# Optimization experiments

Measured on AMD Instinct MI355X. Metric: run time of the kernel, lower is better.

Reference implementation:

```python
import jax, jax.numpy as jnp
import numpy as np
import math

PHI = (1 + math.sqrt(5)) / 2
ALPHA = 1 / PHI          # residual scale
BETA = 1 / PHI ** 2      # sparse-matmul scale
DIM = 1910
NZ = int(DIM * DIM / PHI)


def setup_inputs() -> dict:
    key = jax.random.key(0)
    kx, ki, kv = jax.random.split(key, 3)
    x = jax.random.normal(kx, (8, 4096, DIM), dtype=jnp.float32)
    W_indices = jax.random.randint(ki, (2, NZ), 0, DIM, dtype=jnp.int32)
    W_values = jax.random.normal(kv, (NZ,), dtype=jnp.float32) / math.sqrt(DIM)
    return {"x": x, "W_indices": W_indices, "W_values": W_values}


def reference(x, W_indices, W_values):
    dim = x.shape[-1]
    # COO -> dense: duplicate (row,col) entries sum, matching torch.sparse semantics.
    W = jnp.zeros((dim, dim), dtype=x.dtype).at[W_indices[0], W_indices[1]].add(W_values)
    orig_shape = x.shape
    xf = x.reshape(-1, dim)          # [tokens, dim]
    Wx = xf @ W.T                    # (W @ x.T).T == x @ W.T
    out = ALPHA * xf + BETA * Wx
    return out.reshape(orig_shape)
```

## Files before the change

kernel.cpp:

```cpp
#include <hip/hip_runtime.h>
#include <hip/hip_bf16.h>
#include <stdint.h>

#define DIMV 1910
#define KP   1920
#define NT   30
#define PHI_F  1.6180339887498949f
#define BETA_F 0.3819660112501051f

typedef __attribute__((ext_vector_type(4))) float f32x4;
typedef __attribute__((ext_vector_type(8))) short bf16x8;
typedef __attribute__((ext_vector_type(8))) unsigned short u16x8;

__device__ __forceinline__ void gl16(const void* g, void* l) {
    __builtin_amdgcn_global_load_lds(
        (const __attribute__((address_space(1))) void*)(uintptr_t)g,
        (__attribute__((address_space(3))) void*)(uint32_t)(uintptr_t)l,
        16, 0, 0);
}

__global__ void k_scatter(const int* __restrict__ ridx, const int* __restrict__ cidx,
                          const float* __restrict__ vals, float* __restrict__ Wd, int nz) {
    int i = blockIdx.x * 256 + threadIdx.x;
    if (i < nz) atomicAdd(Wd + (long)ridx[i] * DIMV + cidx[i], vals[i]);
}

__global__ void k_build_w(const float* __restrict__ Wd, unsigned short* __restrict__ Wb, int total8) {
    int stride = gridDim.x * blockDim.x;
    for (int i = blockIdx.x * blockDim.x + threadIdx.x; i < total8; i += stride) {
        int v = i * 8;
        int n = v / KP;
        int k = v - n * KP;
        u16x8 o;
#pragma unroll
        for (int j = 0; j < 8; ++j) {
            int kk = k + j;
            float fv = (n < DIMV && kk < DIMV) ? Wd[(size_t)n * DIMV + kk] : 0.f;
            if (kk == n && n < DIMV) fv += PHI_F;
            __hip_bfloat16 b = __float2bfloat16(fv);
            o[j] = *reinterpret_cast<unsigned short*>(&b);
        }
        *(u16x8*)(Wb + (size_t)v) = o;
    }
}

__global__ void k_conv_x(const float* __restrict__ x, unsigned short* __restrict__ xb, int total8) {
    int stride = gridDim.x * blockDim.x;
    for (int i = blockIdx.x * blockDim.x + threadIdx.x; i < total8; i += stride) {
        int v = i * 8;
        int row = v / KP;
        int col = v - row * KP;
        u16x8 o;
        if (col + 8 <= DIMV) {
            const float2* s = (const float2*)(x + (size_t)row * DIMV + col);
            float2 f0 = s[0], f1 = s[1], f2 = s[2], f3 = s[3];
            float f[8] = {f0.x, f0.y, f1.x, f1.y, f2.x, f2.y, f3.x, f3.y};
#pragma unroll
            for (int j = 0; j < 8; ++j) {
                __hip_bfloat16 b = __float2bfloat16(f[j]);
                o[j] = *reinterpret_cast<unsigned short*>(&b);
            }
        } else {
#pragma unroll
            for (int j = 0; j < 8; ++j) {
                int c = col + j;
                float fv = (c < DIMV) ? x[(size_t)row * DIMV + c] : 0.f;
                __hip_bfloat16 b = __float2bfloat16(fv);
                o[j] = *reinterpret_cast<unsigned short*>(&b);
            }
        }
        *(u16x8*)(xb + (size_t)v) = o;
    }
}

__global__ __launch_bounds__(512, 2) void k_gemm(const short* __restrict__ A,
                                                 const short* __restrict__ B,
                                                 float* __restrict__ C) {
    __shared__ short As[3 * 256 * 64];
    __shared__ short Bs[3 * 128 * 64];

    const int bid = blockIdx.x;
    const int logical = (bid & 7) * 240 + (bid >> 3);
    const int bm = logical / 15;
    const int bn = logical % 15;

    const int tid = threadIdx.x;
    const int w   = tid >> 6;
    const int l   = tid & 63;
    const int wr  = w >> 1;
    const int wc  = w & 1;
    const int fr  = l & 15;
    const int q   = l >> 4;

    const int srow  = tid >> 3;
    const int sslot = (tid & 7) ^ (srow & 7);
    const char* aG = (const char*)A + ((size_t)(bm * 256 + srow) * KP) * 2 + sslot * 16;
    const char* bG = (const char*)B + ((size_t)(bn * 128 + srow) * KP) * 2 + sslot * 16;
    const size_t gstep = (size_t)64 * KP * 2;
    char* aL = (char*)As + tid * 16;
    char* bL = (char*)Bs + tid * 16;

    const int aBase = (wr * 64 + fr) * 128;
    const int bBase = (wc * 64 + fr) * 128;
    const int co0 = ((q    ) ^ (fr & 7)) * 16;
    const int co1 = ((q + 4) ^ (fr & 7)) * 16;

    f32x4 acc[4][4] = {};

#pragma unroll
    for (int g = 0; g < 4; ++g) gl16(aG + g * gstep, aL + g * 8192);
#pragma unroll
    for (int g = 0; g < 2; ++g) gl16(bG + g * gstep, bL + g * 8192);
#pragma unroll
    for (int g = 0; g < 4; ++g) gl16(aG + 128 + g * gstep, aL + 32768 + g * 8192);
#pragma unroll
    for (int g = 0; g < 2; ++g) gl16(bG + 128 + g * gstep, bL + 16384 + g * 8192);
    asm volatile("s_waitcnt vmcnt(6)" ::: "memory");
    __builtin_amdgcn_s_barrier();
    asm volatile("" ::: "memory");

    int aRd = 0, bRd = 0;
    int aSt = 2 * 32768, bSt = 2 * 16384;

#pragma unroll 3
    for (int t = 0; t < NT; ++t) {
        const char* pa = (const char*)As + aRd + aBase;
        const char* pb = (const char*)Bs + bRd + bBase;

        bf16x8 af[4][2], b0[2][2];
#pragma unroll
        for (int mi = 0; mi < 4; ++mi) {
            af[mi][0] = *(const bf16x8*)(pa + mi * 2048 + co0);
            af[mi][1] = *(const bf16x8*)(pa + mi * 2048 + co1);
        }
#pragma unroll
        for (int ni = 0; ni < 2; ++ni) {
            b0[ni][0] = *(const bf16x8*)(pb + ni * 2048 + co0);
            b0[ni][1] = *(const bf16x8*)(pb + ni * 2048 + co1);
        }
        if (t + 2 < NT) {
            const char* g = aG + (size_t)(t + 2) * 128;
#pragma unroll
            for (int gi = 0; gi < 4; ++gi) gl16(g + gi * gstep, aL + aSt + gi * 8192);
        }
        asm volatile("" ::: "memory");
        __builtin_amdgcn_s_barrier();
        asm volatile("" ::: "memory");
        __builtin_amdgcn_s_setprio(1);
#pragma unroll
        for (int mi = 0; mi < 4; ++mi)
#pragma unroll
            for (int ni = 0; ni < 2; ++ni) {
                acc[mi][ni] = __builtin_amdgcn_mfma_f32_16x16x32_bf16(af[mi][0], b0[ni][0], acc[mi][ni], 0, 0, 0);
                acc[mi][ni] = __builtin_amdgcn_mfma_f32_16x16x32_bf16(af[mi][1], b0[ni][1], acc[mi][ni], 0, 0, 0);
            }
        __builtin_amdgcn_s_setprio(0);
        asm volatile("" ::: "memory");
        __builtin_amdgcn_s_barrier();
        asm volatile("" ::: "memory");

        bf16x8 b1[2][2];
#pragma unroll
        for (int ni = 0; ni < 2; ++ni) {
            b1[ni][0] = *(const bf16x8*)(pb + (ni + 2) * 2048 + co0);
            b1[ni][1] = *(const bf16x8*)(pb + (ni + 2) * 2048 + co1);
        }
        if (t + 2 < NT) {
            const char* g = bG + (size_t)(t + 2) * 128;
#pragma unroll
            for (int gi = 0; gi < 2; ++gi) gl16(g + gi * gstep, bL + bSt + gi * 8192);
            asm volatile("s_waitcnt vmcnt(6)" ::: "memory");
        } else {
            asm volatile("s_waitcnt vmcnt(0)" ::: "memory");
        }
        __builtin_amdgcn_s_barrier();
        asm volatile("" ::: "memory");
        __builtin_amdgcn_s_setprio(1);
#pragma unroll
        for (int mi = 0; mi < 4; ++mi)
#pragma unroll
            for (int ni = 0; ni < 2; ++ni) {
                acc[mi][ni + 2] = __builtin_amdgcn_mfma_f32_16x16x32_bf16(af[mi][0], b1[ni][0], acc[mi][ni + 2], 0, 0, 0);
                acc[mi][ni + 2] = __builtin_amdgcn_mfma_f32_16x16x32_bf16(af[mi][1], b1[ni][1], acc[mi][ni + 2], 0, 0, 0);
            }
        __builtin_amdgcn_s_setprio(0);
        asm volatile("" ::: "memory");
        __builtin_amdgcn_s_barrier();
        asm volatile("" ::: "memory");

        aRd += 32768; if (aRd == 98304) aRd = 0;
        bRd += 16384; if (bRd == 49152) bRd = 0;
        aSt += 32768; if (aSt == 98304) aSt = 0;
        bSt += 16384; if (bSt == 49152) bSt = 0;
    }

    const int grow0 = bm * 256 + wr * 64 + q * 4;
    const int gcol0 = bn * 128 + wc * 64 + fr;
#pragma unroll
    for (int mi = 0; mi < 4; ++mi) {
#pragma unroll
        for (int ni = 0; ni < 4; ++ni) {
            int gcol = gcol0 + ni * 16;
            if (gcol < DIMV) {
                size_t base = (size_t)(grow0 + mi * 16) * DIMV + gcol;
#pragma unroll
                for (int r = 0; r < 4; ++r)
                    C[base + (size_t)r * DIMV] = BETA_F * acc[mi][ni][r];
            }
        }
    }
}

extern "C" void kernel_launch(void* const* d_in, const int* in_sizes, int n_in,
                              void* d_out, int out_size, void* d_ws, size_t ws_size,
                              hipStream_t stream) {
    const float* x    = (const float*)d_in[0];
    const int*   widx = (const int*)d_in[1];
    const float* wval = (const float*)d_in[2];
    float* out = (float*)d_out;

    const int nz = in_sizes[2];
    const int M  = in_sizes[0] / DIMV;

    const size_t xb_bytes = (size_t)M * KP * 2;
    const size_t wb_bytes = (size_t)KP * KP * 2;
    const size_t wd_bytes = (size_t)DIMV * DIMV * 4;
    char* ws = (char*)d_ws;
    unsigned short* xb = (unsigned short*)ws;
    unsigned short* Wb = (unsigned short*)(ws + xb_bytes);
    float*          Wd = (float*)(ws + xb_bytes + wb_bytes);
    if (ws_size < xb_bytes + wb_bytes + wd_bytes) return;

    hipMemsetAsync(Wd, 0, wd_bytes, stream);
    k_scatter<<<(nz + 255) / 256, 256, 0, stream>>>(widx, widx + nz, wval, Wd, nz);
    k_build_w<<<1800, 256, 0, stream>>>(Wd, Wb, KP * KP / 8);
    k_conv_x<<<2048, 256, 0, stream>>>(x, xb, M * KP / 8);
    k_gemm<<<1920, 512, 0, stream>>>((const short*)xb, (const short*)Wb, out);
}
```

Measured before the change: 465.3 us.

## Enlarge GEMM tile to 256x256 with 32-wide K stages

Restructures the bf16 MFMA GEMM from 256x128 output tiles with 64-wide K slices to 256x256 tiles with 32-wide K slices. Warps move from a 4x2 to a 2x4 layout, each computing 128x64, and the LDS swizzle is redone for 64-byte rows. The block index mapping is simplified so that neighbouring blocks share the same A rows. The W buffer is padded to 2048 rows to fit the wider tile, and the fp32 scatter scratch now aliases the x workspace. The goal is to raise arithmetic intensity and cut global and LDS traffic per FLOP. The cost is about 7% wasted columns, 128 accumulator registers per lane, and more LDS per block, which may lower occupancy or cause spills.

```diff
diff --git a/kernel.cpp b/kernel.cpp
--- a/kernel.cpp
+++ b/kernel.cpp
@@ -4,7 +4,7 @@
 
 #define DIMV 1910
 #define KP   1920
-#define NT   30
+#define NT   60
 #define PHI_F  1.6180339887498949f
 #define BETA_F 0.3819660112501051f
 
@@ -76,100 +76,86 @@
 __global__ __launch_bounds__(512, 2) void k_gemm(const short* __restrict__ A,
                                                  const short* __restrict__ B,
                                                  float* __restrict__ C) {
-    __shared__ short As[3 * 256 * 64];
-    __shared__ short Bs[3 * 128 * 64];
+    __shared__ short As[3 * 256 * 32];
+    __shared__ short Bs[3 * 256 * 32];
 
     const int bid = blockIdx.x;
-    const int logical = (bid & 7) * 240 + (bid >> 3);
-    const int bm = logical / 15;
-    const int bn = logical % 15;
+    const int bn  = bid & 7;
+    const int bm  = bid >> 3;
 
     const int tid = threadIdx.x;
     const int w   = tid >> 6;
     const int l   = tid & 63;
-    const int wr  = w >> 1;
-    const int wc  = w & 1;
+    const int wm  = w >> 2;
+    const int wn  = w & 3;
     const int fr  = l & 15;
     const int q   = l >> 4;
 
-    const int srow  = tid >> 3;
-    const int sslot = (tid & 7) ^ (srow & 7);
-    const char* aG = (const char*)A + ((size_t)(bm * 256 + srow) * KP) * 2 + sslot * 16;
-    const char* bG = (const char*)B + ((size_t)(bn * 128 + srow) * KP) * 2 + sslot * 16;
-    const size_t gstep = (size_t)64 * KP * 2;
-    char* aL = (char*)As + tid * 16;
-    char* bL = (char*)Bs + tid * 16;
-
-    const int aBase = (wr * 64 + fr) * 128;
-    const int bBase = (wc * 64 + fr) * 128;
-    const int co0 = ((q    ) ^ (fr & 7)) * 16;
-    const int co1 = ((q + 4) ^ (fr & 7)) * 16;
-
-    f32x4 acc[4][4] = {};
-
-#pragma unroll
-    for (int g = 0; g < 4; ++g) gl16(aG + g * gstep, aL + g * 8192);
-#pragma unroll
-    for (int g = 0; g < 2; ++g) gl16(bG + g * gstep, bL + g * 8192);
-#pragma unroll
-    for (int g = 0; g < 4; ++g) gl16(aG + 128 + g * gstep, aL + 32768 + g * 8192);
-#pragma unroll
-    for (int g = 0; g < 2; ++g) gl16(bG + 128 + g * gstep, bL + 16384 + g * 8192);
-    asm volatile("s_waitcnt vmcnt(6)" ::: "memory");
+    const int srow  = tid >> 2;
+    const int lslot = (tid & 3) ^ ((tid >> 3) & 3);
+    const char* aG = (const char*)A + ((size_t)(bm * 256 + srow) * KP) * 2 + lslot * 16;
+    const char* bG = (const char*)B + ((size_t)(bn * 256 + srow) * KP) * 2 + lslot * 16;
+    const size_t gstep = (size_t)128 * KP * 2;
+    char* aL0 = (char*)As + tid * 16;
+    char* bL0 = (char*)Bs + tid * 16;
+
+    const int co    = (q ^ ((fr >> 1) & 3)) * 16;
+    const int aBase = (wm * 128 + fr) * 64 + co;
+    const int bBase = (wn * 64  + fr) * 64 + co;
+
+    f32x4 acc[8][4] = {};
+
+#pragma unroll
+    for (int tt = 0; tt < 2; ++tt) {
+        const char* ga = aG + tt * 64;
+        const char* gb = bG + tt * 64;
+        char* la = aL0 + tt * 16384;
+        char* lb = bL0 + tt * 16384;
+        gl16(ga, la); gl16(ga + gstep, la + 8192);
+        gl16(gb, lb); gl16(gb + gstep, lb + 8192);
+    }
+    asm volatile("s_waitcnt vmcnt(4)" ::: "memory");
     __builtin_amdgcn_s_barrier();
     asm volatile("" ::: "memory");
 
-    int aRd = 0, bRd = 0;
-    int aSt = 2 * 32768, bSt = 2 * 16384;
+    int rdo = 0;
+    int sto = 2 * 16384;
 
 #pragma unroll 3
     for (int t = 0; t < NT; ++t) {
-        const char* pa = (const char*)As + aRd + aBase;
-        const char* pb = (const char*)Bs + bRd + bBase;
-
-        bf16x8 af[4][2], b0[2][2];
-#pragma unroll
-        for (int mi = 0; mi < 4; ++mi) {
-            af[mi][0] = *(const bf16x8*)(pa + mi * 2048 + co0);
-            af[mi][1] = *(const bf16x8*)(pa + mi * 2048 + co1);
-        }
-#pragma unroll
-        for (int ni = 0; ni < 2; ++ni) {
-            b0[ni][0] = *(const bf16x8*)(pb + ni * 2048 + co0);
-            b0[ni][1] = *(const bf16x8*)(pb + ni * 2048 + co1);
-        }
+        const char* pa = (const char*)As + rdo + aBase;
+        const char* pb = (const char*)Bs + rdo + bBase;
+
+        bf16x8 af[8], b01[2];
+#pragma unroll
+        for (int mi = 0; mi < 8; ++mi) af[mi] = *(const bf16x8*)(pa + mi * 1024);
+#pragma unroll
+        for (int ni = 0; ni < 2; ++ni) b01[ni] = *(const bf16x8*)(pb + ni * 1024);
         if (t + 2 < NT) {
-            const char* g = aG + (size_t)(t + 2) * 128;
-#pragma unroll
-            for (int gi = 0; gi < 4; ++gi) gl16(g + gi * gstep, aL + aSt + gi * 8192);
+            const char* g = aG + (size_t)(t + 2) * 64;
+            gl16(g, aL0 + sto); gl16(g + gstep, aL0 + sto + 8192);
         }
         asm volatile("" ::: "memory");
         __builtin_amdgcn_s_barrier();
         asm volatile("" ::: "memory");
         __builtin_amdgcn_s_setprio(1);
 #pragma unroll
-        for (int mi = 0; mi < 4; ++mi)
-#pragma unroll
-            for (int ni = 0; ni < 2; ++ni) {
-                acc[mi][ni] = __builtin_amdgcn_mfma_f32_16x16x32_bf16(af[mi][0], b0[ni][0], acc[mi][ni], 0, 0, 0);
-                acc[mi][ni] = __builtin_amdgcn_mfma_f32_16x16x32_bf16(af[mi][1], b0[ni][1], acc[mi][ni], 0, 0, 0);
-            }
+        for (int mi = 0; mi < 8; ++mi)
+#pragma unroll
+            for (int ni = 0; ni < 2; ++ni)
+                acc[mi][ni] = __builtin_amdgcn_mfma_f32_16x16x32_bf16(af[mi], b01[ni], acc[mi][ni], 0, 0, 0);
         __builtin_amdgcn_s_setprio(0);
         asm volatile("" ::: "memory");
         __builtin_amdgcn_s_barrier();
         asm volatile("" ::: "memory");
 
-        bf16x8 b1[2][2];
-#pragma unroll
-        for (int ni = 0; ni < 2; ++ni) {
-            b1[ni][0] = *(const bf16x8*)(pb + (ni + 2) * 2048 + co0);
-            b1[ni][1] = *(const bf16x8*)(pb + (ni + 2) * 2048 + co1);
-        }
+        bf16x8 b23[2];
+#pragma unroll
+        for (int ni = 0; ni < 2; ++ni) b23[ni] = *(const bf16x8*)(pb + (ni + 2) * 1024);
         if (t + 2 < NT) {
-            const char* g = bG + (size_t)(t + 2) * 128;
-#pragma unroll
-            for (int gi = 0; gi < 2; ++gi) gl16(g + gi * gstep, bL + bSt + gi * 8192);
-            asm volatile("s_waitcnt vmcnt(6)" ::: "memory");
+            const char* g = bG + (size_t)(t + 2) * 64;
+            gl16(g, bL0 + sto); gl16(g + gstep, bL0 + sto + 8192);
+            asm volatile("s_waitcnt vmcnt(4)" ::: "memory");
         } else {
             asm volatile("s_waitcnt vmcnt(0)" ::: "memory");
         }
@@ -177,27 +163,23 @@
         asm volatile("" ::: "memory");
         __builtin_amdgcn_s_setprio(1);
 #pragma unroll
-        for (int mi = 0; mi < 4; ++mi)
-#pragma unroll
-            for (int ni = 0; ni < 2; ++ni) {
-                acc[mi][ni + 2] = __builtin_amdgcn_mfma_f32_16x16x32_bf16(af[mi][0], b1[ni][0], acc[mi][ni + 2], 0, 0, 0);
-                acc[mi][ni + 2] = __builtin_amdgcn_mfma_f32_16x16x32_bf16(af[mi][1], b1[ni][1], acc[mi][ni + 2], 0, 0, 0);
-            }
+        for (int mi = 0; mi < 8; ++mi)
+#pragma unroll
+            for (int ni = 0; ni < 2; ++ni)
+                acc[mi][ni + 2] = __builtin_amdgcn_mfma_f32_16x16x32_bf16(af[mi], b23[ni], acc[mi][ni + 2], 0, 0, 0);
         __builtin_amdgcn_s_setprio(0);
         asm volatile("" ::: "memory");
         __builtin_amdgcn_s_barrier();
         asm volatile("" ::: "memory");
 
-        aRd += 32768; if (aRd == 98304) aRd = 0;
-        bRd += 16384; if (bRd == 49152) bRd = 0;
-        aSt += 32768; if (aSt == 98304) aSt = 0;
-        bSt += 16384; if (bSt == 49152) bSt = 0;
-    }
-
-    const int grow0 = bm * 256 + wr * 64 + q * 4;
-    const int gcol0 = bn * 128 + wc * 64 + fr;
-#pragma unroll
-    for (int mi = 0; mi < 4; ++mi) {
+        rdo += 16384; if (rdo == 49152) rdo = 0;
+        sto += 16384; if (sto == 49152) sto = 0;
+    }
+
+    const int grow0 = bm * 256 + wm * 128 + q * 4;
+    const int gcol0 = bn * 256 + wn * 64 + fr;
+#pragma unroll
+    for (int mi = 0; mi < 8; ++mi) {
 #pragma unroll
         for (int ni = 0; ni < 4; ++ni) {
             int gcol = gcol0 + ni * 16;
@@ -223,17 +205,18 @@
     const int M  = in_sizes[0] / DIMV;
 
     const size_t xb_bytes = (size_t)M * KP * 2;
-    const size_t wb_bytes = (size_t)KP * KP * 2;
+    const size_t wb_bytes = (size_t)2048 * KP * 2;
     const size_t wd_bytes = (size_t)DIMV * DIMV * 4;
     char* ws = (char*)d_ws;
     unsigned short* xb = (unsigned short*)ws;
     unsigned short* Wb = (unsigned short*)(ws + xb_bytes);
-    float*          Wd = (float*)(ws + xb_bytes + wb_bytes);
-    if (ws_size < xb_bytes + wb_bytes + wd_bytes) return;
+    float*          Wd = (float*)ws;
+    if (ws_size < xb_bytes + wb_bytes) return;
+    (void)wd_bytes;
 
     hipMemsetAsync(Wd, 0, wd_bytes, stream);
     k_scatter<<<(nz + 255) / 256, 256, 0, stream>>>(widx, widx + nz, wval, Wd, nz);
     k_build_w<<<1800, 256, 0, stream>>>(Wd, Wb, KP * KP / 8);
     k_conv_x<<<2048, 256, 0, stream>>>(x, xb, M * KP / 8);
-    k_gemm<<<1920, 512, 0, stream>>>((const short*)xb, (const short*)Wb, out);
-}
+    k_gemm<<<1024, 512, 0, stream>>>((const short*)xb, (const short*)Wb, out);
+}
```

After: 477.2 us. 2.6% more time.
